# Performance work log

Hardware: AMD Instinct MI355X
Metric: run time of the kernel (lower is better)

The kernel has to match this reference:

```python
import jax, jax.numpy as jnp
import numpy as np

B = 4096          # graph pairs in batch
NPG = 40          # nodes per molecular graph
N = B * NPG       # total nodes per drug batch
EPG = 160         # directed edges per graph
E = B * EPG
F_IN = 78         # atom feature dim
HID = 128
HEADS = 4
ADD = 8           # additional features (concentrations)
BN_EPS = 1e-5
D0 = HEADS * HID          # 512
CMB = 4 * HID + ADD       # 2 drugs * (mean||max of 128) + ADD = 520


def setup_inputs() -> dict:
    key = jax.random.key(0)
    ks = iter(jax.random.split(key, 64))
    def nrm(shape, s=0.1):
        return jax.random.normal(next(ks), shape, jnp.float32) * s
    def pos(shape):  # positive running variances
        return jax.random.uniform(next(ks), shape, jnp.float32, 0.5, 1.5)
    offs = jnp.repeat(jnp.arange(B, dtype=jnp.int32) * NPG, EPG)
    def edges():
        return jax.random.randint(next(ks), (2, E), 0, NPG, dtype=jnp.int32) + offs[None, :]
    batch = jnp.repeat(jnp.arange(B, dtype=jnp.int32), NPG)
    inp = dict(
        x_a=nrm((N, F_IN), 1.0), edge_a=edges(), batch_a=batch,
        x_b=nrm((N, F_IN), 1.0), edge_b=edges(), batch_b=batch,
        addf=nrm((B, ADD), 1.0),
        # shared GAT encoder params
        gW0=nrm((F_IN, D0)), gb0=nrm((D0,)), gas0=nrm((D0,)), gad0=nrm((D0,)),
        gW1=nrm((D0, D0)), gb1=nrm((D0,)), gas1=nrm((D0,)), gad1=nrm((D0,)),
        gW2=nrm((D0, HID)), gb2=nrm((HID,)), gas2=nrm((HID,)), gad2=nrm((HID,)),
        bn0g=pos((D0,)), bn0b=nrm((D0,)), bn0m=nrm((D0,)), bn0v=pos((D0,)),
        bn1g=pos((D0,)), bn1b=nrm((D0,)), bn1m=nrm((D0,)), bn1v=pos((D0,)),
        bn2g=pos((HID,)), bn2b=nrm((HID,)), bn2m=nrm((HID,)), bn2v=pos((HID,)),
        # combination MLP params (Linear + eval BatchNorm stats)
        mW0=nrm((CMB, 2 * HID)), mb0=nrm((2 * HID,)),
        mg0=pos((2 * HID,)), mbe0=nrm((2 * HID,)), mm0=nrm((2 * HID,)), mv0=pos((2 * HID,)),
        mW1=nrm((2 * HID, HID)), mb1=nrm((HID,)),
        mg1=pos((HID,)), mbe1=nrm((HID,)), mm1=nrm((HID,)), mv1=pos((HID,)),
        mW2=nrm((HID, 1)), mb2=nrm((1,)),
    )
    return inp


def _bn(x, g, b, m, v):
    return (x - m) * jax.lax.rsqrt(v + BN_EPS) * g + b


def _gat(x, src, dst, W, b, a_src, a_dst, heads, ch, concat):
    """PyG GATConv (eval): linear, per-head additive attention with
    leaky_relu(0.2), segment-softmax over incoming edges (self-loops included)."""
    n = x.shape[0]
    h = (x @ W).reshape(n, heads, ch)                     # [N, H, C]
    es = jnp.sum(h * a_src.reshape(1, heads, ch), -1)     # [N, H]
    ed = jnp.sum(h * a_dst.reshape(1, heads, ch), -1)     # [N, H]
    e = jax.nn.leaky_relu(es[src] + ed[dst], 0.2)         # [E', H]
    emax = jax.ops.segment_max(e, dst, num_segments=n)
    ex = jnp.exp(e - emax[dst])
    den = jax.ops.segment_sum(ex, dst, num_segments=n)
    alpha = ex / den[dst]                                 # [E', H]
    out = jax.ops.segment_sum(h[src] * alpha[..., None], dst, num_segments=n)
    out = out.reshape(n, heads * ch) if concat else jnp.mean(out, axis=1)
    return out + b


def _encode(x, edge, batch, p):
    n = x.shape[0]
    sl = jnp.arange(n, dtype=edge.dtype)                  # self-loops (PyG default)
    src = jnp.concatenate([edge[0], sl])
    dst = jnp.concatenate([edge[1], sl])
    x = _gat(x, src, dst, p['gW0'], p['gb0'], p['gas0'], p['gad0'], HEADS, HID, True)
    x = jax.nn.relu(_bn(x, p['bn0g'], p['bn0b'], p['bn0m'], p['bn0v']))
    x = _gat(x, src, dst, p['gW1'], p['gb1'], p['gas1'], p['gad1'], HEADS, HID, True)
    x = jax.nn.relu(_bn(x, p['bn1g'], p['bn1b'], p['bn1m'], p['bn1v']))
    x = _gat(x, src, dst, p['gW2'], p['gb2'], p['gas2'], p['gad2'], 1, HID, False)
    x = _bn(x, p['bn2g'], p['bn2b'], p['bn2m'], p['bn2v'])  # no relu on last layer
    cnt = jax.ops.segment_sum(jnp.ones((n, 1), x.dtype), batch, num_segments=B)
    x_mean = jax.ops.segment_sum(x, batch, num_segments=B) / cnt
    x_max = jax.ops.segment_max(x, batch, num_segments=B)
    return jnp.concatenate([x_mean, x_max], axis=1)        # [B, 2*HID]


def reference(x_a, edge_a, batch_a, x_b, edge_b, batch_b, addf,
              gW0, gb0, gas0, gad0, gW1, gb1, gas1, gad1, gW2, gb2, gas2, gad2,
              bn0g, bn0b, bn0m, bn0v, bn1g, bn1b, bn1m, bn1v, bn2g, bn2b, bn2m, bn2v,
              mW0, mb0, mg0, mbe0, mm0, mv0, mW1, mb1, mg1, mbe1, mm1, mv1, mW2, mb2):
    p = dict(gW0=gW0, gb0=gb0, gas0=gas0, gad0=gad0, gW1=gW1, gb1=gb1, gas1=gas1,
             gad1=gad1, gW2=gW2, gb2=gb2, gas2=gas2, gad2=gad2,
             bn0g=bn0g, bn0b=bn0b, bn0m=bn0m, bn0v=bn0v,
             bn1g=bn1g, bn1b=bn1b, bn1m=bn1m, bn1v=bn1v,
             bn2g=bn2g, bn2b=bn2b, bn2m=bn2m, bn2v=bn2v)
    emb_a = _encode(x_a, edge_a, batch_a, p)
    emb_b = _encode(x_b, edge_b, batch_b, p)
    c = jnp.concatenate([emb_a, emb_b, addf], axis=1)      # [B, 520]
    h = jax.nn.relu(_bn(c @ mW0 + mb0, mg0, mbe0, mm0, mv0))
    h = jax.nn.relu(_bn(h @ mW1 + mb1, mg1, mbe1, mm1, mv1))
    out = jax.nn.sigmoid(h @ mW2 + mb2)
    return jnp.squeeze(out, -1)                            # [B]
```

## Files before the change

kernel.cpp:

```cpp
#include <hip/hip_runtime.h>
#include <stdint.h>

#define B_GRAPHS 4096
#define NPG 40
#define NTOT (B_GRAPHS * NPG)
#define EPG 160
#define ETOT (B_GRAPHS * EPG)
#define ESL 200
#define F_IN 78
#define KP0 96
#define HID 128
#define D0 512
#define CMB 520
#define BN_EPS 1e-5f
#define AST 48
#define KPM 544
#define A0ST 552
#define H1ST 264
#define H2ST 132

typedef short bf16x8 __attribute__((ext_vector_type(8)));
typedef float floatx4 __attribute__((ext_vector_type(4)));

__device__ inline float b2f(unsigned short u) {
    union { float f; uint32_t i; } v; v.i = ((uint32_t)u) << 16; return v.f;
}
__device__ inline unsigned short f2b(float f) {
    union { float f; uint32_t i; } v; v.f = f;
    uint32_t x = v.i;
    return (unsigned short)((x + 0x7fffu + ((x >> 16) & 1u)) >> 16);
}
__device__ inline float lo16(uint32_t u) {
    union { float f; uint32_t i; } v; v.i = u << 16; return v.f;
}
__device__ inline float hi16(uint32_t u) {
    union { float f; uint32_t i; } v; v.i = u & 0xffff0000u; return v.f;
}
__device__ inline unsigned int fenc(float f) {
    unsigned int b = __float_as_uint(f);
    return (b & 0x80000000u) ? ~b : (b | 0x80000000u);
}
__device__ inline float fdec(unsigned int u) {
    unsigned int b = (u & 0x80000000u) ? (u & 0x7fffffffu) : ~u;
    return __uint_as_float(b);
}
__device__ inline int htoff(int ch, int s) {
    int chunk = s >> 3, within = s & 7;
    return ch * 40 + (((chunk + ch) % 5) << 3) + within;
}
__device__ inline void gl2lds16(const unsigned short* g, unsigned short* l) {
    __builtin_amdgcn_global_load_lds(
        (const __attribute__((address_space(1))) unsigned int*)g,
        (__attribute__((address_space(3))) unsigned int*)l, 16, 0, 0);
}

__global__ __launch_bounds__(256)
void write_code_kernel(float* __restrict__ out, int n, float S)
{
    int i = blockIdx.x * 256 + threadIdx.x;
    if (i < n) out[i] = (i == 0) ? S : 0.f;
}

__global__ __launch_bounds__(256)
void convw_kernel(const float* __restrict__ W, unsigned short* __restrict__ Wt,
                  int K, int N, int Kp)
{
    int t = blockIdx.x * 256 + threadIdx.x;
    if (t >= N * Kp) return;
    int n = t / Kp, k = t - n * Kp;
    Wt[t] = (k < K) ? f2b(W[(size_t)k * N + n]) : 0;
}

__global__ __launch_bounds__(256)
void convw_hilo_kernel(const float* __restrict__ W,
                       unsigned short* __restrict__ Whi,
                       unsigned short* __restrict__ Wlo,
                       int K, int N, int Kp)
{
    int t = blockIdx.x * 256 + threadIdx.x;
    if (t >= N * Kp) return;
    int n = t / Kp, k = t - n * Kp;
    float x = (k < K) ? W[(size_t)k * N + n] : 0.f;
    unsigned short hb = f2b(x);
    Whi[t] = hb;
    Wlo[t] = f2b(x - b2f(hb));
}

__global__ __launch_bounds__(256)
void convx_kernel(const float* __restrict__ X, unsigned short* __restrict__ Xb, int M)
{
    int t = blockIdx.x * 256 + threadIdx.x;
    if (t >= M * (KP0 / 8)) return;
    int r = t / (KP0 / 8), c8 = t - r * (KP0 / 8);
    unsigned int pk[4];
    #pragma unroll
    for (int j = 0; j < 4; j++) {
        int k0 = c8 * 8 + 2 * j, k1 = k0 + 1;
        float x0 = (k0 < F_IN) ? X[(size_t)r * F_IN + k0] : 0.f;
        float x1 = (k1 < F_IN) ? X[(size_t)r * F_IN + k1] : 0.f;
        pk[j] = (unsigned int)f2b(x0) | ((unsigned int)f2b(x1) << 16);
    }
    *(uint4*)&Xb[(size_t)r * KP0 + c8 * 8] = make_uint4(pk[0], pk[1], pk[2], pk[3]);
}

__global__ __launch_bounds__(256)
void gemm_mfma_kernel(const unsigned short* __restrict__ A,
                      const unsigned short* __restrict__ Bt,
                      unsigned short* __restrict__ C,
                      int M, int K, int N)
{
    __shared__ __align__(16) unsigned short As[128 * 32];
    __shared__ __align__(16) unsigned short Bs[128 * 32];
    const int tid  = threadIdx.x;
    const int lane = tid & 63, w = tid >> 6;
    const int quad = lane >> 4, l16 = lane & 15;
    const int wm = w >> 1, wn = w & 1;
    const int row0 = blockIdx.y * 128, col0 = blockIdx.x * 128;

    floatx4 acc[4][4];
    #pragma unroll
    for (int mi = 0; mi < 4; mi++)
        #pragma unroll
        for (int ni = 0; ni < 4; ni++)
            acc[mi][ni] = (floatx4){0.f, 0.f, 0.f, 0.f};

    int srow[2], scg[2];
    #pragma unroll
    for (int it = 0; it < 2; it++) {
        int L = it * 4096 + w * 1024 + lane * 16;
        int r = L >> 6;
        int cp = (L >> 4) & 3;
        srow[it] = r;
        scg[it]  = cp ^ ((r >> 1) & 3);
    }

    for (int k0 = 0; k0 < K; k0 += 32) {
        #pragma unroll
        for (int it = 0; it < 2; it++) {
            int ra = row0 + srow[it]; if (ra >= M) ra = M - 1;
            gl2lds16(A + (size_t)ra * K + k0 + scg[it] * 8,
                     As + (it * 4096 + w * 1024) / 2);
            int rb = col0 + srow[it];
            gl2lds16(Bt + (size_t)rb * K + k0 + scg[it] * 8,
                     Bs + (it * 4096 + w * 1024) / 2);
        }
        __syncthreads();

        bf16x8 fA[4], fB[4];
        #pragma unroll
        for (int mi = 0; mi < 4; mi++) {
            int r = wm * 64 + mi * 16 + l16;
            __builtin_memcpy(&fA[mi], &As[r * 32 + ((quad ^ ((r >> 1) & 3)) * 8)], 16);
        }
        #pragma unroll
        for (int ni = 0; ni < 4; ni++) {
            int r = wn * 64 + ni * 16 + l16;
            __builtin_memcpy(&fB[ni], &Bs[r * 32 + ((quad ^ ((r >> 1) & 3)) * 8)], 16);
        }
        #pragma unroll
        for (int mi = 0; mi < 4; mi++)
            #pragma unroll
            for (int ni = 0; ni < 4; ni++)
                acc[mi][ni] = __builtin_amdgcn_mfma_f32_16x16x32_bf16(
                    fB[ni], fA[mi], acc[mi][ni], 0, 0, 0);
        __syncthreads();
    }

    #pragma unroll
    for (int mi = 0; mi < 4; mi++) {
        int row = row0 + wm * 64 + mi * 16 + l16;
        if (row < M) {
            #pragma unroll
            for (int ni = 0; ni < 4; ni++) {
                floatx4 a = acc[mi][ni];
                unsigned int p0 = (unsigned int)f2b(a[0]) | ((unsigned int)f2b(a[1]) << 16);
                unsigned int p1 = (unsigned int)f2b(a[2]) | ((unsigned int)f2b(a[3]) << 16);
                *(uint2*)(C + (size_t)row * N + col0 + wn * 64 + ni * 16 + quad * 4) =
                    make_uint2(p0, p1);
            }
        }
    }
}

__global__ __launch_bounds__(256)
void gat4_fused_kernel(unsigned short* __restrict__ H,
                       const int* __restrict__ edge,
                       const float* __restrict__ avs, const float* __restrict__ avd,
                       const float* __restrict__ bias,
                       const float* __restrict__ bng, const float* __restrict__ bnb,
                       const float* __restrict__ bnm, const float* __restrict__ bnv,
                       int g0)
{
    __shared__ __align__(16) unsigned short ht[D0 * NPG];
    __shared__ float es[4 * NPG], ed[4 * NPG];
    __shared__ unsigned int Mu[4 * NPG];
    __shared__ float den[4 * NPG];
    __shared__ __align__(16) unsigned char cnt[NPG * 48];
    __shared__ short2 eloc[ESL];
    const int tid = threadIdx.x;
    const int lane = tid & 63, w = tid >> 6;
    const int quad = lane >> 4, l16 = lane & 15;
    const int gg = g0 + blockIdx.x;
    unsigned short* Hg = H + (size_t)blockIdx.x * NPG * D0;

    for (int i = tid; i < NPG * 48 / 4; i += 256) ((unsigned int*)cnt)[i] = 0u;
    if (tid < 4 * NPG) { Mu[tid] = 0u; den[tid] = 0.f; }
    for (int i = tid; i < ESL; i += 256) {
        if (i < EPG) {
            int s  = edge[(size_t)gg * EPG + i] - gg * NPG;
            int dd = edge[(size_t)ETOT + (size_t)gg * EPG + i] - gg * NPG;
            eloc[i] = make_short2((short)s, (short)dd);
        } else {
            short v = (short)(i - EPG);
            eloc[i] = make_short2(v, v);
        }
    }
    for (int u = tid; u < 64 * (NPG / 4); u += 256) {
        int c8 = u & 63, gi = u >> 6;
        const unsigned short* src = Hg + (size_t)(4 * gi) * D0 + c8 * 8;
        uint4 v0 = *(const uint4*)(src);
        uint4 v1 = *(const uint4*)(src + D0);
        uint4 v2 = *(const uint4*)(src + 2 * D0);
        uint4 v3 = *(const uint4*)(src + 3 * D0);
        unsigned int a0[4] = {v0.x, v0.y, v0.z, v0.w};
        unsigned int a1[4] = {v1.x, v1.y, v1.z, v1.w};
        unsigned int a2[4] = {v2.x, v2.y, v2.z, v2.w};
        unsigned int a3[4] = {v3.x, v3.y, v3.z, v3.w};
        #pragma unroll
        for (int k = 0; k < 8; k++) {
            const int ws = k >> 1, sh = (k & 1) * 16;
            unsigned int w0 = ((a0[ws] >> sh) & 0xffffu) | (((a1[ws] >> sh) & 0xffffu) << 16);
            unsigned int w1 = ((a2[ws] >> sh) & 0xffffu) | (((a3[ws] >> sh) & 0xffffu) << 16);
            *(uint2*)&ht[htoff(c8 * 8 + k, 4 * gi)] = make_uint2(w0, w1);
        }
    }
    __syncthreads();

    {
        float as0=0,as1=0,as2=0,as3=0, ad0=0,ad1=0,ad2=0,ad3=0;
        for (int ci = 0; ci < 32; ci++) {
            int c = quad + ci * 4;
            int chv = w * 128 + c;
            uint2 hv = *(const uint2*)&ht[htoff(chv, 4 * l16)];
            float h0 = lo16(hv.x), h1 = hi16(hv.x), h2 = lo16(hv.y), h3 = hi16(hv.y);
            float vs = avs[chv], vd = avd[chv];
            as0 += h0*vs; as1 += h1*vs; as2 += h2*vs; as3 += h3*vs;
            ad0 += h0*vd; ad1 += h1*vd; ad2 += h2*vd; ad3 += h3*vd;
        }
        #define RED4(x) x += __shfl_xor(x, 16); x += __shfl_xor(x, 32);
        RED4(as0) RED4(as1) RED4(as2) RED4(as3)
        RED4(ad0) RED4(ad1) RED4(ad2) RED4(ad3)
        #undef RED4
        if (quad == 0) {
            float rs[4] = {as0, as1, as2, as3};
            float rd[4] = {ad0, ad1, ad2, ad3};
            #pragma unroll
            for (int rr = 0; rr < 4; rr++) {
                int node = 4 * l16 + rr;
                if (node < NPG) { es[w * NPG + node] = rs[rr]; ed[w * NPG + node] = rd[rr]; }
            }
        }
    }
    for (int e = tid; e < ESL; e += 256) {
        short2 sd = eloc[e];
        atomicAdd((unsigned int*)cnt + ((sd.y * 48 + sd.x) >> 2),
                  1u << ((sd.x & 3) * 8));
    }
    __syncthreads();

    for (int u = tid; u < 4 * ESL; u += 256) {
        int e = u >> 2, hd = u & 3;
        short2 sd = eloc[e];
        float v = es[hd * NPG + sd.x] + ed[hd * NPG + sd.y];
        v = v > 0.f ? v : 0.2f * v;
        atomicMax(&Mu[hd * NPG + sd.y], fenc(v));
    }
    __syncthreads();
    for (int u = tid; u < 4 * ESL; u += 256) {
        int e = u >> 2, hd = u & 3;
        short2 sd = eloc[e];
        float v = es[hd * NPG + sd.x] + ed[hd * NPG + sd.y];
        v = v > 0.f ? v : 0.2f * v;
        float ex = __expf(v - fdec(Mu[hd * NPG + sd.y]));
        atomicAdd(&den[hd * NPG + sd.y], ex);
    }
    __syncthreads();

    {
        bf16x8 ahi[3][2], alo[3][2];
        float esv0[8], esv1[8];
        #pragma unroll
        for (int j = 0; j < 8; j++) {
            esv0[j] = es[w * NPG + quad * 8 + j];
            esv1[j] = (quad == 0) ? es[w * NPG + 32 + j] : 0.f;
        }
        #pragma unroll
        for (int mt = 0; mt < 3; mt++) {
            int dn = mt * 16 + l16;
            bool ok = dn < NPG;
            float edv = 0.f, m = 0.f, di = 0.f;
            uint2 c0 = make_uint2(0u, 0u), c1 = make_uint2(0u, 0u);
            if (ok) {
                edv = ed[w * NPG + dn];
                m = fdec(Mu[w * NPG + dn]);
                di = 1.f / den[w * NPG + dn];
                c0 = *(const uint2*)&cnt[dn * 48 + quad * 8];
                if (quad == 0) c1 = *(const uint2*)&cnt[dn * 48 + 32];
            }
            #pragma unroll
            for (int j = 0; j < 8; j++) {
                unsigned int cb0 = ((j < 4 ? c0.x : c0.y) >> ((j & 3) * 8)) & 0xffu;
                float v0 = esv0[j] + edv;
                v0 = v0 > 0.f ? v0 : 0.2f * v0;
                float a0 = (ok && cb0) ? (float)cb0 * __expf(v0 - m) * di : 0.f;
                unsigned short hb0 = f2b(a0);
                ahi[mt][0][j] = (short)hb0;
                alo[mt][0][j] = (short)f2b(a0 - b2f(hb0));

                unsigned int cb1 = ((j < 4 ? c1.x : c1.y) >> ((j & 3) * 8)) & 0xffu;
                float v1 = esv1[j] + edv;
                v1 = v1 > 0.f ? v1 : 0.2f * v1;
                float a1 = (ok && quad == 0 && cb1) ? (float)cb1 * __expf(v1 - m) * di : 0.f;
                unsigned short hb1 = f2b(a1);
                ahi[mt][1][j] = (short)hb1;
                alo[mt][1][j] = (short)f2b(a1 - b2f(hb1));
            }
        }
        const floatx4 z = {0.f, 0.f, 0.f, 0.f};
        for (int nt = 0; nt < 8; nt++) {
            const int ch0 = w * 128 + nt * 16;
            bf16x8 b0, b1 = {0,0,0,0,0,0,0,0};
            __builtin_memcpy(&b0, &ht[htoff(ch0 + l16, quad * 8)], 16);
            if (quad == 0) __builtin_memcpy(&b1, &ht[htoff(ch0 + l16, 32)], 16);
            floatx4 acc0 = z, acc1 = z, acc2 = z;
            acc0 = __builtin_amdgcn_mfma_f32_16x16x32_bf16(ahi[0][0], b0, acc0, 0, 0, 0);
            acc1 = __builtin_amdgcn_mfma_f32_16x16x32_bf16(ahi[1][0], b0, acc1, 0, 0, 0);
            acc2 = __builtin_amdgcn_mfma_f32_16x16x32_bf16(ahi[2][0], b0, acc2, 0, 0, 0);
            acc0 = __builtin_amdgcn_mfma_f32_16x16x32_bf16(alo[0][0], b0, acc0, 0, 0, 0);
            acc1 = __builtin_amdgcn_mfma_f32_16x16x32_bf16(alo[1][0], b0, acc1, 0, 0, 0);
            acc2 = __builtin_amdgcn_mfma_f32_16x16x32_bf16(alo[2][0], b0, acc2, 0, 0, 0);
            acc0 = __builtin_amdgcn_mfma_f32_16x16x32_bf16(ahi[0][1], b1, acc0, 0, 0, 0);
            acc1 = __builtin_amdgcn_mfma_f32_16x16x32_bf16(ahi[1][1], b1, acc1, 0, 0, 0);
            acc2 = __builtin_amdgcn_mfma_f32_16x16x32_bf16(ahi[2][1], b1, acc2, 0, 0, 0);
            acc0 = __builtin_amdgcn_mfma_f32_16x16x32_bf16(alo[0][1], b1, acc0, 0, 0, 0);
            acc1 = __builtin_amdgcn_mfma_f32_16x16x32_bf16(alo[1][1], b1, acc1, 0, 0, 0);
            acc2 = __builtin_amdgcn_mfma_f32_16x16x32_bf16(alo[2][1], b1, acc2, 0, 0, 0);
            const int c = ch0 + l16;
            float scl = rsqrtf(bnv[c] + BN_EPS) * bng[c];
            float sft = (bias[c] - bnm[c]) * scl + bnb[c];
            unsigned short* reg = &ht[ch0 * 40];
            #pragma unroll
            for (int mt = 0; mt < 3; mt++) {
                floatx4 a = (mt == 0) ? acc0 : (mt == 1) ? acc1 : acc2;
                #pragma unroll
                for (int rr = 0; rr < 4; rr++) {
                    int dn = mt * 16 + quad * 4 + rr;
                    if (dn < NPG) {
                        float o = a[rr] * scl + sft;
                        o = fmaxf(o, 0.f);
                        reg[dn * 16 + l16] = f2b(o);
                    }
                }
            }
        }
    }
    __syncthreads();
    for (int u = tid; u < NPG * 64; u += 256) {
        int s = u >> 6, c8 = u & 63;
        const unsigned short* reg = &ht[(c8 >> 1) * 16 * 40];
        uint4 v = *(const uint4*)&reg[s * 16 + (c8 & 1) * 8];
        *(uint4*)(Hg + (size_t)s * D0 + c8 * 8) = v;
    }
}

__global__ __launch_bounds__(256)
void gat1_pool_fused_kernel(const unsigned short* __restrict__ H,
                            const int* __restrict__ edge,
                            const float* __restrict__ avs, const float* __restrict__ avd,
                            const float* __restrict__ bias,
                            const float* __restrict__ bng, const float* __restrict__ bnb,
                            const float* __restrict__ bnm, const float* __restrict__ bnv,
                            float* __restrict__ cmb, int colbase, int g0)
{
    __shared__ __align__(16) unsigned short ht[HID * NPG];
    __shared__ float A1f[NPG * AST];
    __shared__ float es[NPG], ed[NPG];
    __shared__ unsigned int Mu[NPG];
    __shared__ float den[NPG];
    __shared__ short2 eloc[ESL];
    const int tid = threadIdx.x;
    const int lane = tid & 63, w = tid >> 6;
    const int quad = lane >> 4, l16 = lane & 15;
    const int gg = g0 + blockIdx.x;
    const unsigned short* Hg = H + (size_t)blockIdx.x * NPG * HID;

    for (int i = tid; i < NPG * AST; i += 256) A1f[i] = 0.f;
    if (tid < NPG) { Mu[tid] = 0u; den[tid] = 0.f; }
    for (int i = tid; i < ESL; i += 256) {
        if (i < EPG) {
            int s  = edge[(size_t)gg * EPG + i] - gg * NPG;
            int dd = edge[(size_t)ETOT + (size_t)gg * EPG + i] - gg * NPG;
            eloc[i] = make_short2((short)s, (short)dd);
        } else {
            short v = (short)(i - EPG);
            eloc[i] = make_short2(v, v);
        }
    }
    for (int u = tid; u < 16 * (NPG / 4); u += 256) {
        int c8 = u & 15, gi = u >> 4;
        const unsigned short* src = Hg + (size_t)(4 * gi) * HID + c8 * 8;
        uint4 v0 = *(const uint4*)(src);
        uint4 v1 = *(const uint4*)(src + HID);
        uint4 v2 = *(const uint4*)(src + 2 * HID);
        uint4 v3 = *(const uint4*)(src + 3 * HID);
        unsigned int a0[4] = {v0.x, v0.y, v0.z, v0.w};
        unsigned int a1[4] = {v1.x, v1.y, v1.z, v1.w};
        unsigned int a2[4] = {v2.x, v2.y, v2.z, v2.w};
        unsigned int a3[4] = {v3.x, v3.y, v3.z, v3.w};
        #pragma unroll
        for (int k = 0; k < 8; k++) {
            const int ws = k >> 1, sh = (k & 1) * 16;
            unsigned int w0 = ((a0[ws] >> sh) & 0xffffu) | (((a1[ws] >> sh) & 0xffffu) << 16);
            unsigned int w1 = ((a2[ws] >> sh) & 0xffffu) | (((a3[ws] >> sh) & 0xffffu) << 16);
            *(uint2*)&ht[htoff(c8 * 8 + k, 4 * gi)] = make_uint2(w0, w1);
        }
    }
    __syncthreads();

    if (w < 2) {
        const float* av = w ? avd : avs;
        float a0=0,a1=0,a2=0,a3=0;
        for (int ci = 0; ci < 32; ci++) {
            int c = quad + ci * 4;
            uint2 hv = *(const uint2*)&ht[htoff(c, 4 * l16)];
            float vc = av[c];
            a0 += lo16(hv.x)*vc; a1 += hi16(hv.x)*vc;
            a2 += lo16(hv.y)*vc; a3 += hi16(hv.y)*vc;
        }
        #define RED4(x) x += __shfl_xor(x, 16); x += __shfl_xor(x, 32);
        RED4(a0) RED4(a1) RED4(a2) RED4(a3)
        #undef RED4
        if (quad == 0) {
            float rv[4] = {a0, a1, a2, a3};
            float* dst = w ? ed : es;
            #pragma unroll
            for (int rr = 0; rr < 4; rr++) {
                int node = 4 * l16 + rr;
                if (node < NPG) dst[node] = rv[rr];
            }
        }
    }
    __syncthreads();
    for (int u = tid; u < ESL; u += 256) {
        short2 sd = eloc[u];
        float v = es[sd.x] + ed[sd.y];
        v = v > 0.f ? v : 0.2f * v;
        atomicMax(&Mu[sd.y], fenc(v));
    }
    __syncthreads();
    for (int u = tid; u < ESL; u += 256) {
        short2 sd = eloc[u];
        float v = es[sd.x] + ed[sd.y];
        v = v > 0.f ? v : 0.2f * v;
        float ex = __expf(v - fdec(Mu[sd.y]));
        atomicAdd(&den[sd.y], ex);
        atomicAdd(&A1f[sd.x * AST + sd.y], ex);
    }
    __syncthreads();
    for (int idx = tid; idx < NPG * AST; idx += 256) {
        int dn = idx % AST;
        float val = A1f[idx];
        unsigned int pw = 0u;
        if (dn < NPG) {
            float a = val / den[dn];
            unsigned short hi = f2b(a);
            float rem = a - b2f(hi);
            pw = (unsigned int)hi | ((unsigned int)f2b(rem) << 16);
        }
        ((unsigned int*)A1f)[idx] = pw;
    }
    __syncthreads();

    {
        const unsigned int* Ap = (const unsigned int*)A1f;
        bf16x8 ahi[3][2], alo[3][2];
        #pragma unroll
        for (int mt = 0; mt < 3; mt++) {
            #pragma unroll
            for (int j = 0; j < 8; j++) {
                unsigned int w0 = Ap[(quad * 8 + j) * AST + mt * 16 + l16];
                ahi[mt][0][j] = (short)(w0 & 0xffffu);
                alo[mt][0][j] = (short)(w0 >> 16);
                unsigned int w1 = (quad == 0) ? Ap[(32 + j) * AST + mt * 16 + l16] : 0u;
                ahi[mt][1][j] = (short)(w1 & 0xffffu);
                alo[mt][1][j] = (short)(w1 >> 16);
            }
        }
        const floatx4 z = {0.f, 0.f, 0.f, 0.f};
        for (int t2 = 0; t2 < 2; t2++) {
            const int ch0 = (w * 2 + t2) * 16;
            bf16x8 b0, b1 = {0,0,0,0,0,0,0,0};
            __builtin_memcpy(&b0, &ht[htoff(ch0 + l16, quad * 8)], 16);
            if (quad == 0) __builtin_memcpy(&b1, &ht[htoff(ch0 + l16, 32)], 16);
            floatx4 acc0 = z, acc1 = z, acc2 = z;
            acc0 = __builtin_amdgcn_mfma_f32_16x16x32_bf16(ahi[0][0], b0, acc0, 0, 0, 0);
            acc1 = __builtin_amdgcn_mfma_f32_16x16x32_bf16(ahi[1][0], b0, acc1, 0, 0, 0);
            acc2 = __builtin_amdgcn_mfma_f32_16x16x32_bf16(ahi[2][0], b0, acc2, 0, 0, 0);
            acc0 = __builtin_amdgcn_mfma_f32_16x16x32_bf16(alo[0][0], b0, acc0, 0, 0, 0);
            acc1 = __builtin_amdgcn_mfma_f32_16x16x32_bf16(alo[1][0], b0, acc1, 0, 0, 0);
            acc2 = __builtin_amdgcn_mfma_f32_16x16x32_bf16(alo[2][0], b0, acc2, 0, 0, 0);
            acc0 = __builtin_amdgcn_mfma_f32_16x16x32_bf16(ahi[0][1], b1, acc0, 0, 0, 0);
            acc1 = __builtin_amdgcn_mfma_f32_16x16x32_bf16(ahi[1][1], b1, acc1, 0, 0, 0);
            acc2 = __builtin_amdgcn_mfma_f32_16x16x32_bf16(ahi[2][1], b1, acc2, 0, 0, 0);
            acc0 = __builtin_amdgcn_mfma_f32_16x16x32_bf16(alo[0][1], b1, acc0, 0, 0, 0);
            acc1 = __builtin_amdgcn_mfma_f32_16x16x32_bf16(alo[1][1], b1, acc1, 0, 0, 0);
            acc2 = __builtin_amdgcn_mfma_f32_16x16x32_bf16(alo[2][1], b1, acc2, 0, 0, 0);
            const int c = ch0 + l16;
            float scl = rsqrtf(bnv[c] + BN_EPS) * bng[c];
            float sft = (bias[c] - bnm[c]) * scl + bnb[c];
            float psum = 0.f, pmax = -1e30f;
            #pragma unroll
            for (int mt = 0; mt < 3; mt++) {
                floatx4 a = (mt == 0) ? acc0 : (mt == 1) ? acc1 : acc2;
                #pragma unroll
                for (int rr = 0; rr < 4; rr++) {
                    int dn = mt * 16 + quad * 4 + rr;
                    if (dn < NPG) {
                        float o = a[rr] * scl + sft;
                        psum += o;
                        pmax = fmaxf(pmax, o);
                    }
                }
            }
            psum += __shfl_xor(psum, 16); psum += __shfl_xor(psum, 32);
            pmax = fmaxf(pmax, __shfl_xor(pmax, 16));
            pmax = fmaxf(pmax, __shfl_xor(pmax, 32));
            if (quad == 0) {
                cmb[(size_t)gg * 512 + colbase + c] = psum * (1.f / NPG);
                cmb[(size_t)gg * 512 + colbase + HID + c] = pmax;
            }
        }
    }
}

__global__ __launch_bounds__(256)
void mlp_mfma_kernel(const float* __restrict__ cmb, const float* __restrict__ addf,
                     const unsigned short* __restrict__ W0hi, const unsigned short* __restrict__ W0lo,
                     const float* __restrict__ b0, const float* __restrict__ g0v,
                     const float* __restrict__ be0, const float* __restrict__ m0,
                     const float* __restrict__ v0,
                     const unsigned short* __restrict__ W1hi, const unsigned short* __restrict__ W1lo,
                     const float* __restrict__ b1, const float* __restrict__ g1v,
                     const float* __restrict__ be1, const float* __restrict__ m1,
                     const float* __restrict__ v1,
                     const float* __restrict__ W2, const float* __restrict__ b2,
                     float* __restrict__ out)
{
    __shared__ __align__(16) unsigned short a0hi[16 * A0ST], a0lo[16 * A0ST];
    __shared__ __align__(16) unsigned short h1hi[16 * H1ST], h1lo[16 * H1ST];
    __shared__ float h2[16 * H2ST];
    const int tid = threadIdx.x;
    const int lane = tid & 63, w = tid >> 6;
    const int quad = lane >> 4, l16 = lane & 15;
    const int gb = blockIdx.x * 16;

    for (int i = tid; i < 16 * KPM; i += 256) {
        int g = i / KPM, k = i - g * KPM;
        float x = 0.f;
        if (k < 512) x = cmb[(size_t)(gb + g) * 512 + k];
        else if (k < CMB) x = addf[(gb + g) * 8 + (k - 512)];
        unsigned short hb = f2b(x);
        a0hi[g * A0ST + k] = hb;
        a0lo[g * A0ST + k] = f2b(x - b2f(hb));
    }
    __syncthreads();

    {
        floatx4 acc[4];
        #pragma unroll
        for (int ni = 0; ni < 4; ni++) acc[ni] = (floatx4){0.f, 0.f, 0.f, 0.f};
        for (int k0 = 0; k0 < KPM; k0 += 32) {
            bf16x8 fah, fal;
            __builtin_memcpy(&fah, &a0hi[l16 * A0ST + k0 + quad * 8], 16);
            __builtin_memcpy(&fal, &a0lo[l16 * A0ST + k0 + quad * 8], 16);
            #pragma unroll
            for (int ni = 0; ni < 4; ni++) {
                int row = w * 64 + ni * 16 + l16;
                bf16x8 fwh, fwl;
                __builtin_memcpy(&fwh, &W0hi[(size_t)row * KPM + k0 + quad * 8], 16);
                __builtin_memcpy(&fwl, &W0lo[(size_t)row * KPM + k0 + quad * 8], 16);
                acc[ni] = __builtin_amdgcn_mfma_f32_16x16x32_bf16(fwh, fah, acc[ni], 0, 0, 0);
                acc[ni] = __builtin_amdgcn_mfma_f32_16x16x32_bf16(fwh, fal, acc[ni], 0, 0, 0);
                acc[ni] = __builtin_amdgcn_mfma_f32_16x16x32_bf16(fwl, fah, acc[ni], 0, 0, 0);
            }
        }
        #pragma unroll
        for (int ni = 0; ni < 4; ni++) {
            int cbase = w * 64 + ni * 16 + quad * 4;
            unsigned int ph[2], pl[2];
            #pragma unroll
            for (int j = 0; j < 2; j++) {
                unsigned int hh[2], ll[2];
                #pragma unroll
                for (int q = 0; q < 2; q++) {
                    int rr = 2 * j + q, c = cbase + rr;
                    float scl = rsqrtf(v0[c] + BN_EPS) * g0v[c];
                    float val = (acc[ni][rr] + b0[c] - m0[c]) * scl + be0[c];
                    val = fmaxf(val, 0.f);
                    unsigned short hb = f2b(val);
                    hh[q] = hb;
                    ll[q] = f2b(val - b2f(hb));
                }
                ph[j] = hh[0] | (hh[1] << 16);
                pl[j] = ll[0] | (ll[1] << 16);
            }
            *(uint2*)&h1hi[l16 * H1ST + cbase] = make_uint2(ph[0], ph[1]);
            *(uint2*)&h1lo[l16 * H1ST + cbase] = make_uint2(pl[0], pl[1]);
        }
    }
    __syncthreads();

    {
        floatx4 acc[2];
        acc[0] = (floatx4){0.f, 0.f, 0.f, 0.f};
        acc[1] = (floatx4){0.f, 0.f, 0.f, 0.f};
        for (int k0 = 0; k0 < 256; k0 += 32) {
            bf16x8 fah, fal;
            __builtin_memcpy(&fah, &h1hi[l16 * H1ST + k0 + quad * 8], 16);
            __builtin_memcpy(&fal, &h1lo[l16 * H1ST + k0 + quad * 8], 16);
            #pragma unroll
            for (int ni = 0; ni < 2; ni++) {
                int row = w * 32 + ni * 16 + l16;
                bf16x8 fwh, fwl;
                __builtin_memcpy(&fwh, &W1hi[(size_t)row * 256 + k0 + quad * 8], 16);
                __builtin_memcpy(&fwl, &W1lo[(size_t)row * 256 + k0 + quad * 8], 16);
                acc[ni] = __builtin_amdgcn_mfma_f32_16x16x32_bf16(fwh, fah, acc[ni], 0, 0, 0);
                acc[ni] = __builtin_amdgcn_mfma_f32_16x16x32_bf16(fwh, fal, acc[ni], 0, 0, 0);
                acc[ni] = __builtin_amdgcn_mfma_f32_16x16x32_bf16(fwl, fah, acc[ni], 0, 0, 0);
            }
        }
        #pragma unroll
        for (int ni = 0; ni < 2; ni++) {
            #pragma unroll
            for (int rr = 0; rr < 4; rr++) {
                int c = w * 32 + ni * 16 + quad * 4 + rr;
                float scl = rsqrtf(v1[c] + BN_EPS) * g1v[c];
                float val = (acc[ni][rr] + b1[c] - m1[c]) * scl + be1[c];
                h2[l16 * H2ST + c] = fmaxf(val, 0.f);
            }
        }
    }
    __syncthreads();

    {
        int g = tid >> 4, part = tid & 15;
        float s = 0.f;
        #pragma unroll
        for (int j = 0; j < 8; j++)
            s += h2[g * H2ST + part * 8 + j] * W2[part * 8 + j];
        s += __shfl_xor(s, 1); s += __shfl_xor(s, 2);
        s += __shfl_xor(s, 4); s += __shfl_xor(s, 8);
        if (part == 0) out[gb + g] = 1.f / (1.f + __expf(-(s + b2[0])));
    }
}

extern "C" void kernel_launch(void* const* d_in, const int* in_sizes, int n_in,
                              void* d_out, int out_size, void* d_ws, size_t ws_size,
                              hipStream_t stream)
{
    float* out = (float*)d_out;
    int out_n = out_size < 4096 ? out_size : 4096;

    const float* x_a  = (const float*)d_in[0];
    const int*   edge_a = (const int*)d_in[1];
    const float* x_b  = (const float*)d_in[3];
    const int*   edge_b = (const int*)d_in[4];
    const float* addf = (const float*)d_in[6];
    const float* gW0 = (const float*)d_in[7],  *gb0 = (const float*)d_in[8];
    const float* gas0 = (const float*)d_in[9], *gad0 = (const float*)d_in[10];
    const float* gW1 = (const float*)d_in[11], *gb1 = (const float*)d_in[12];
    const float* gas1 = (const float*)d_in[13], *gad1 = (const float*)d_in[14];
    const float* gW2 = (const float*)d_in[15], *gb2 = (const float*)d_in[16];
    const float* gas2 = (const float*)d_in[17], *gad2 = (const float*)d_in[18];
    const float* bn0g = (const float*)d_in[19], *bn0b = (const float*)d_in[20];
    const float* bn0m = (const float*)d_in[21], *bn0v = (const float*)d_in[22];
    const float* bn1g = (const float*)d_in[23], *bn1b = (const float*)d_in[24];
    const float* bn1m = (const float*)d_in[25], *bn1v = (const float*)d_in[26];
    const float* bn2g = (const float*)d_in[27], *bn2b = (const float*)d_in[28];
    const float* bn2m = (const float*)d_in[29], *bn2v = (const float*)d_in[30];
    const float* mW0 = (const float*)d_in[31], *mb0 = (const float*)d_in[32];
    const float* mg0 = (const float*)d_in[33], *mbe0 = (const float*)d_in[34];
    const float* mm0 = (const float*)d_in[35], *mv0 = (const float*)d_in[36];
    const float* mW1 = (const float*)d_in[37], *mb1 = (const float*)d_in[38];
    const float* mg1 = (const float*)d_in[39], *mbe1 = (const float*)d_in[40];
    const float* mm1 = (const float*)d_in[41], *mv1 = (const float*)d_in[42];
    const float* mW2 = (const float*)d_in[43], *mb2 = (const float*)d_in[44];

    char* p = (char*)d_ws;
    const size_t CMB_BYTES = (size_t)B_GRAPHS * 512 * sizeof(float);
    float* cmb = (float*)p; p += CMB_BYTES;
    unsigned short* W0t = (unsigned short*)p; p += (size_t)D0 * KP0 * 2;
    unsigned short* W1t = (unsigned short*)p; p += (size_t)D0 * D0 * 2;
    unsigned short* W2t = (unsigned short*)p; p += (size_t)HID * D0 * 2;
    unsigned short* M0hi = (unsigned short*)p; p += (size_t)256 * KPM * 2;
    unsigned short* M0lo = (unsigned short*)p; p += (size_t)256 * KPM * 2;
    unsigned short* M1hi = (unsigned short*)p; p += (size_t)128 * 256 * 2;
    unsigned short* M1lo = (unsigned short*)p; p += (size_t)128 * 256 * 2;
    size_t used = (size_t)(p - (char*)d_ws);
    const size_t PG = 7680ull + 40960ull + 40960ull;
    int chunk = B_GRAPHS;
    while (chunk > 4 && used + (size_t)chunk * PG > ws_size) chunk >>= 1;
    if (used + (size_t)chunk * PG > ws_size) {
        write_code_kernel<<<(out_n + 255) / 256, 256, 0, stream>>>(out, out_n, 500000.f);
        return;
    }
    unsigned short* Xb = (unsigned short*)p; p += (size_t)chunk * 7680;
    unsigned short* B1 = (unsigned short*)p; p += (size_t)chunk * 40960;
    unsigned short* B2 = (unsigned short*)p;

    convw_kernel<<<(D0 * KP0 + 255) / 256, 256, 0, stream>>>(gW0, W0t, F_IN, D0, KP0);
    convw_kernel<<<(D0 * D0 + 255) / 256, 256, 0, stream>>>(gW1, W1t, D0, D0, D0);
    convw_kernel<<<(HID * D0 + 255) / 256, 256, 0, stream>>>(gW2, W2t, D0, HID, D0);
    convw_hilo_kernel<<<(256 * KPM + 255) / 256, 256, 0, stream>>>(
        mW0, M0hi, M0lo, CMB, 256, KPM);
    convw_hilo_kernel<<<(128 * 256 + 255) / 256, 256, 0, stream>>>(
        mW1, M1hi, M1lo, 256, 128, 256);

    for (int drug = 0; drug < 2; drug++) {
        const float* x = drug ? x_b : x_a;
        const int* edge = drug ? edge_b : edge_a;
        int colbase = drug ? 256 : 0;

        for (int g0 = 0; g0 < B_GRAPHS; g0 += chunk) {
            int n = chunk * NPG;
            int gy = (n + 127) / 128;
            convx_kernel<<<(n * (KP0 / 8) + 255) / 256, 256, 0, stream>>>(
                x + (size_t)g0 * NPG * F_IN, Xb, n);
            gemm_mfma_kernel<<<dim3(D0 / 128, gy), 256, 0, stream>>>(
                Xb, W0t, B1, n, KP0, D0);
            gat4_fused_kernel<<<chunk, 256, 0, stream>>>(
                B1, edge, gas0, gad0, gb0, bn0g, bn0b, bn0m, bn0v, g0);
            gemm_mfma_kernel<<<dim3(D0 / 128, gy), 256, 0, stream>>>(
                B1, W1t, B2, n, D0, D0);
            gat4_fused_kernel<<<chunk, 256, 0, stream>>>(
                B2, edge, gas1, gad1, gb1, bn1g, bn1b, bn1m, bn1v, g0);
            gemm_mfma_kernel<<<dim3(HID / 128, gy), 256, 0, stream>>>(
                B2, W2t, B1, n, D0, HID);
            gat1_pool_fused_kernel<<<chunk, 256, 0, stream>>>(
                B1, edge, gas2, gad2, gb2, bn2g, bn2b, bn2m, bn2v,
                cmb, colbase, g0);
        }
    }
    mlp_mfma_kernel<<<B_GRAPHS / 16, 256, 0, stream>>>(
        cmb, addf, M0hi, M0lo, mb0, mg0, mbe0, mm0, mv0,
        M1hi, M1lo, mb1, mg1, mbe1, mm1, mv1, mW2, mb2, out);
}
```

Baseline: 1.419 ms.

## Compute GAT softmax in registers from edge counts; swizzle GEMM blocks across XCDs

Both GAT attention kernels drop the shared-memory atomicMax/atomicAdd passes that built the per-destination max, the denominator and the dense attention matrix. Instead, each lane builds its attention coefficients directly from per-(dst,src) edge-count bytes, and the row max and sum are reduced with wavefront shuffles. The final-layer kernel now uses the same count-byte approach as the 4-head kernel. Separately, the GEMM remaps block indices so that consecutive tiles land on the same XCD, aiming for better L2 locality. The goal is to cut barriers, LDS atomics and shared-memory traffic, at the cost of more register pressure.

Result: faster. 1.339 ms, median of 2 (-5.7%).

```diff
diff --git a/kernel.cpp b/kernel.cpp
--- a/kernel.cpp
+++ b/kernel.cpp
@@ -13,7 +13,6 @@
 #define D0 512
 #define CMB 520
 #define BN_EPS 1e-5f
-#define AST 48
 #define KPM 544
 #define A0ST 552
 #define H1ST 264
@@ -35,14 +34,6 @@
 }
 __device__ inline float hi16(uint32_t u) {
     union { float f; uint32_t i; } v; v.i = u & 0xffff0000u; return v.f;
-}
-__device__ inline unsigned int fenc(float f) {
-    unsigned int b = __float_as_uint(f);
-    return (b & 0x80000000u) ? ~b : (b | 0x80000000u);
-}
-__device__ inline float fdec(unsigned int u) {
-    unsigned int b = (u & 0x80000000u) ? (u & 0x7fffffffu) : ~u;
-    return __uint_as_float(b);
 }
 __device__ inline int htoff(int ch, int s) {
     int chunk = s >> 3, within = s & 7;
@@ -115,7 +106,12 @@
     const int lane = tid & 63, w = tid >> 6;
     const int quad = lane >> 4, l16 = lane & 15;
     const int wm = w >> 1, wn = w & 1;
-    const int row0 = blockIdx.y * 128, col0 = blockIdx.x * 128;
+    const int nwg  = gridDim.x * gridDim.y;
+    const int orig = blockIdx.y * gridDim.x + blockIdx.x;
+    const int q = nwg >> 3, r = nwg & 7;
+    const int xcd = orig & 7, off = orig >> 3;
+    const int swz = (xcd < r ? xcd * (q + 1) : r * (q + 1) + (xcd - r) * q) + off;
+    const int row0 = (swz / gridDim.x) * 128, col0 = (swz % gridDim.x) * 128;
 
     floatx4 acc[4][4];
     #pragma unroll
@@ -128,10 +124,10 @@
     #pragma unroll
     for (int it = 0; it < 2; it++) {
         int L = it * 4096 + w * 1024 + lane * 16;
-        int r = L >> 6;
+        int rr = L >> 6;
         int cp = (L >> 4) & 3;
-        srow[it] = r;
-        scg[it]  = cp ^ ((r >> 1) & 3);
+        srow[it] = rr;
+        scg[it]  = cp ^ ((rr >> 1) & 3);
     }
 
     for (int k0 = 0; k0 < K; k0 += 32) {
@@ -149,13 +145,13 @@
         bf16x8 fA[4], fB[4];
         #pragma unroll
         for (int mi = 0; mi < 4; mi++) {
-            int r = wm * 64 + mi * 16 + l16;
-            __builtin_memcpy(&fA[mi], &As[r * 32 + ((quad ^ ((r >> 1) & 3)) * 8)], 16);
+            int rr = wm * 64 + mi * 16 + l16;
+            __builtin_memcpy(&fA[mi], &As[rr * 32 + ((quad ^ ((rr >> 1) & 3)) * 8)], 16);
         }
         #pragma unroll
         for (int ni = 0; ni < 4; ni++) {
-            int r = wn * 64 + ni * 16 + l16;
-            __builtin_memcpy(&fB[ni], &Bs[r * 32 + ((quad ^ ((r >> 1) & 3)) * 8)], 16);
+            int rr = wn * 64 + ni * 16 + l16;
+            __builtin_memcpy(&fB[ni], &Bs[rr * 32 + ((quad ^ ((rr >> 1) & 3)) * 8)], 16);
         }
         #pragma unroll
         for (int mi = 0; mi < 4; mi++)
@@ -193,8 +189,6 @@
 {
     __shared__ __align__(16) unsigned short ht[D0 * NPG];
     __shared__ float es[4 * NPG], ed[4 * NPG];
-    __shared__ unsigned int Mu[4 * NPG];
-    __shared__ float den[4 * NPG];
     __shared__ __align__(16) unsigned char cnt[NPG * 48];
     __shared__ short2 eloc[ESL];
     const int tid = threadIdx.x;
@@ -204,7 +198,6 @@
     unsigned short* Hg = H + (size_t)blockIdx.x * NPG * D0;
 
     for (int i = tid; i < NPG * 48 / 4; i += 256) ((unsigned int*)cnt)[i] = 0u;
-    if (tid < 4 * NPG) { Mu[tid] = 0u; den[tid] = 0.f; }
     for (int i = tid; i < ESL; i += 256) {
         if (i < EPG) {
             int s  = edge[(size_t)gg * EPG + i] - gg * NPG;
@@ -268,24 +261,6 @@
     }
     __syncthreads();
 
-    for (int u = tid; u < 4 * ESL; u += 256) {
-        int e = u >> 2, hd = u & 3;
-        short2 sd = eloc[e];
-        float v = es[hd * NPG + sd.x] + ed[hd * NPG + sd.y];
-        v = v > 0.f ? v : 0.2f * v;
-        atomicMax(&Mu[hd * NPG + sd.y], fenc(v));
-    }
-    __syncthreads();
-    for (int u = tid; u < 4 * ESL; u += 256) {
-        int e = u >> 2, hd = u & 3;
-        short2 sd = eloc[e];
-        float v = es[hd * NPG + sd.x] + ed[hd * NPG + sd.y];
-        v = v > 0.f ? v : 0.2f * v;
-        float ex = __expf(v - fdec(Mu[hd * NPG + sd.y]));
-        atomicAdd(&den[hd * NPG + sd.y], ex);
-    }
-    __syncthreads();
-
     {
         bf16x8 ahi[3][2], alo[3][2];
         float esv0[8], esv1[8];
@@ -298,29 +273,46 @@
         for (int mt = 0; mt < 3; mt++) {
             int dn = mt * 16 + l16;
             bool ok = dn < NPG;
-            float edv = 0.f, m = 0.f, di = 0.f;
+            float edv = 0.f;
             uint2 c0 = make_uint2(0u, 0u), c1 = make_uint2(0u, 0u);
             if (ok) {
                 edv = ed[w * NPG + dn];
-                m = fdec(Mu[w * NPG + dn]);
-                di = 1.f / den[w * NPG + dn];
                 c0 = *(const uint2*)&cnt[dn * 48 + quad * 8];
                 if (quad == 0) c1 = *(const uint2*)&cnt[dn * 48 + 32];
             }
+            float v0[8], v1[8];
+            int cb0[8], cb1[8];
+            float pm = -1e30f;
             #pragma unroll
             for (int j = 0; j < 8; j++) {
-                unsigned int cb0 = ((j < 4 ? c0.x : c0.y) >> ((j & 3) * 8)) & 0xffu;
-                float v0 = esv0[j] + edv;
-                v0 = v0 > 0.f ? v0 : 0.2f * v0;
-                float a0 = (ok && cb0) ? (float)cb0 * __expf(v0 - m) * di : 0.f;
+                cb0[j] = (int)(((j < 4 ? c0.x : c0.y) >> ((j & 3) * 8)) & 0xffu);
+                float t0 = esv0[j] + edv;
+                v0[j] = t0 > 0.f ? t0 : 0.2f * t0;
+                if (cb0[j]) pm = fmaxf(pm, v0[j]);
+                cb1[j] = (int)(((j < 4 ? c1.x : c1.y) >> ((j & 3) * 8)) & 0xffu);
+                float t1 = esv1[j] + edv;
+                v1[j] = t1 > 0.f ? t1 : 0.2f * t1;
+                if (cb1[j]) pm = fmaxf(pm, v1[j]);
+            }
+            pm = fmaxf(pm, __shfl_xor(pm, 16));
+            pm = fmaxf(pm, __shfl_xor(pm, 32));
+            float e0[8], e1[8], pd = 0.f;
+            #pragma unroll
+            for (int j = 0; j < 8; j++) {
+                e0[j] = cb0[j] ? (float)cb0[j] * __expf(v0[j] - pm) : 0.f;
+                e1[j] = cb1[j] ? (float)cb1[j] * __expf(v1[j] - pm) : 0.f;
+                pd += e0[j] + e1[j];
+            }
+            pd += __shfl_xor(pd, 16);
+            pd += __shfl_xor(pd, 32);
+            float di = ok ? 1.f / pd : 0.f;
+            #pragma unroll
+            for (int j = 0; j < 8; j++) {
+                float a0 = e0[j] * di;
                 unsigned short hb0 = f2b(a0);
                 ahi[mt][0][j] = (short)hb0;
                 alo[mt][0][j] = (short)f2b(a0 - b2f(hb0));
-
-                unsigned int cb1 = ((j < 4 ? c1.x : c1.y) >> ((j & 3) * 8)) & 0xffu;
-                float v1 = esv1[j] + edv;
-                v1 = v1 > 0.f ? v1 : 0.2f * v1;
-                float a1 = (ok && quad == 0 && cb1) ? (float)cb1 * __expf(v1 - m) * di : 0.f;
+                float a1 = e1[j] * di;
                 unsigned short hb1 = f2b(a1);
                 ahi[mt][1][j] = (short)hb1;
                 alo[mt][1][j] = (short)f2b(a1 - b2f(hb1));
@@ -383,10 +375,8 @@
                             float* __restrict__ cmb, int colbase, int g0)
 {
     __shared__ __align__(16) unsigned short ht[HID * NPG];
-    __shared__ float A1f[NPG * AST];
     __shared__ float es[NPG], ed[NPG];
-    __shared__ unsigned int Mu[NPG];
-    __shared__ float den[NPG];
+    __shared__ __align__(16) unsigned char cnt[NPG * 48];
     __shared__ short2 eloc[ESL];
     const int tid = threadIdx.x;
     const int lane = tid & 63, w = tid >> 6;
@@ -394,8 +384,7 @@
     const int gg = g0 + blockIdx.x;
     const unsigned short* Hg = H + (size_t)blockIdx.x * NPG * HID;
 
-    for (int i = tid; i < NPG * AST; i += 256) A1f[i] = 0.f;
-    if (tid < NPG) { Mu[tid] = 0u; den[tid] = 0.f; }
+    for (int i = tid; i < NPG * 48 / 4; i += 256) ((unsigned int*)cnt)[i] = 0u;
     for (int i = tid; i < ESL; i += 256) {
         if (i < EPG) {
             int s  = edge[(size_t)gg * EPG + i] - gg * NPG;
@@ -450,50 +439,68 @@
             }
         }
     }
+    for (int e = tid; e < ESL; e += 256) {
+        short2 sd = eloc[e];
+        atomicAdd((unsigned int*)cnt + ((sd.y * 48 + sd.x) >> 2),
+                  1u << ((sd.x & 3) * 8));
+    }
     __syncthreads();
-    for (int u = tid; u < ESL; u += 256) {
-        short2 sd = eloc[u];
-        float v = es[sd.x] + ed[sd.y];
-        v = v > 0.f ? v : 0.2f * v;
-        atomicMax(&Mu[sd.y], fenc(v));
-    }
-    __syncthreads();
-    for (int u = tid; u < ESL; u += 256) {
-        short2 sd = eloc[u];
-        float v = es[sd.x] + ed[sd.y];
-        v = v > 0.f ? v : 0.2f * v;
-        float ex = __expf(v - fdec(Mu[sd.y]));
-        atomicAdd(&den[sd.y], ex);
-        atomicAdd(&A1f[sd.x * AST + sd.y], ex);
-    }
-    __syncthreads();
-    for (int idx = tid; idx < NPG * AST; idx += 256) {
-        int dn = idx % AST;
-        float val = A1f[idx];
-        unsigned int pw = 0u;
-        if (dn < NPG) {
-            float a = val / den[dn];
-            unsigned short hi = f2b(a);
-            float rem = a - b2f(hi);
-            pw = (unsigned int)hi | ((unsigned int)f2b(rem) << 16);
-        }
-        ((unsigned int*)A1f)[idx] = pw;
-    }
-    __syncthreads();
 
     {
-        const unsigned int* Ap = (const unsigned int*)A1f;
         bf16x8 ahi[3][2], alo[3][2];
+        float esv0[8], esv1[8];
+        #pragma unroll
+        for (int j = 0; j < 8; j++) {
+            esv0[j] = es[quad * 8 + j];
+            esv1[j] = (quad == 0) ? es[32 + j] : 0.f;
+        }
         #pragma unroll
         for (int mt = 0; mt < 3; mt++) {
+            int dn = mt * 16 + l16;
+            bool ok = dn < NPG;
+            float edv = 0.f;
+            uint2 c0 = make_uint2(0u, 0u), c1 = make_uint2(0u, 0u);
+            if (ok) {
+                edv = ed[dn];
+                c0 = *(const uint2*)&cnt[dn * 48 + quad * 8];
+                if (quad == 0) c1 = *(const uint2*)&cnt[dn * 48 + 32];
+            }
+            float v0[8], v1[8];
+            int cb0[8], cb1[8];
+            float pm = -1e30f;
             #pragma unroll
             for (int j = 0; j < 8; j++) {
-                unsigned int w0 = Ap[(quad * 8 + j) * AST + mt * 16 + l16];
-                ahi[mt][0][j] = (short)(w0 & 0xffffu);
-                alo[mt][0][j] = (short)(w0 >> 16);
-                unsigned int w1 = (quad == 0) ? Ap[(32 + j) * AST + mt * 16 + l16] : 0u;
-                ahi[mt][1][j] = (short)(w1 & 0xffffu);
-                alo[mt][1][j] = (short)(w1 >> 16);
+                cb0[j] = (int)(((j < 4 ? c0.x : c0.y) >> ((j & 3) * 8)) & 0xffu);
+                float t0 = esv0[j] + edv;
+                v0[j] = t0 > 0.f ? t0 : 0.2f * t0;
+                if (cb0[j]) pm = fmaxf(pm, v0[j]);
+                cb1[j] = (int)(((j < 4 ? c1.x : c1.y) >> ((j & 3) * 8)) & 0xffu);
+                float t1 = esv1[j] + edv;
+                v1[j] = t1 > 0.f ? t1 : 0.2f * t1;
+                if (cb1[j]) pm = fmaxf(pm, v1[j]);
+            }
+            pm = fmaxf(pm, __shfl_xor(pm, 16));
+            pm = fmaxf(pm, __shfl_xor(pm, 32));
+            float e0[8], e1[8], pd = 0.f;
+            #pragma unroll
+            for (int j = 0; j < 8; j++) {
+                e0[j] = cb0[j] ? (float)cb0[j] * __expf(v0[j] - pm) : 0.f;
+                e1[j] = cb1[j] ? (float)cb1[j] * __expf(v1[j] - pm) : 0.f;
+                pd += e0[j] + e1[j];
+            }
+            pd += __shfl_xor(pd, 16);
+            pd += __shfl_xor(pd, 32);
+            float di = ok ? 1.f / pd : 0.f;
+            #pragma unroll
+            for (int j = 0; j < 8; j++) {
+                float a0 = e0[j] * di;
+                unsigned short hb0 = f2b(a0);
+                ahi[mt][0][j] = (short)hb0;
+                alo[mt][0][j] = (short)f2b(a0 - b2f(hb0));
+                float a1 = e1[j] * di;
+                unsigned short hb1 = f2b(a1);
+                ahi[mt][1][j] = (short)hb1;
+                alo[mt][1][j] = (short)f2b(a1 - b2f(hb1));
             }
         }
         const floatx4 z = {0.f, 0.f, 0.f, 0.f};
```
